# Optimization experiments

Measured on AMD Instinct MI355X. Metric: run time of the kernel, lower is better.

## Reference

```python
import jax, jax.numpy as jnp
import numpy as np

N = 100000
E = 1600000
D_PCA = 50
D_BIO = 64
HID = 32
HEADS = 4
OUT = 50
EPS = 1e-5


def setup_inputs() -> dict:
    key = jax.random.key(0)
    ks = jax.random.split(key, 32)
    g = lambda i, shape, s=0.05: jax.random.normal(ks[i], shape, dtype=jnp.float32) * s
    inp = {
        'x_pca': jax.random.normal(ks[0], (N, D_PCA), dtype=jnp.float32),
        'x_bio': jax.random.normal(ks[1], (N, D_BIO), dtype=jnp.float32),
        'edge_index': jax.random.randint(ks[2], (2, E), 0, N, dtype=jnp.int32),
        # bio encoder: Linear(64,16) -> BN(16) -> ELU -> Linear(16,16) -> ELU
        'bioW1': g(3, (16, D_BIO)), 'biob1': g(4, (16,)),
        'bn0_g': 1.0 + g(5, (16,)), 'bn0_b': g(6, (16,)),
        'bn0_m': g(7, (16,)), 'bn0_v': 1.0 + 0.1 * jax.random.uniform(ks[8], (16,), dtype=jnp.float32),
        'bioW2': g(9, (16, 16)), 'biob2': g(10, (16,)),
        # GATv2 layer 1: in = 50+16 = 66, out = HEADS*HID concat
        'Wl1': g(11, (HEADS * HID, D_PCA + 16)), 'bl1': g(12, (HEADS * HID,)),
        'Wr1': g(13, (HEADS * HID, D_PCA + 16)), 'br1': g(14, (HEADS * HID,)),
        'att1': g(15, (HEADS, HID)), 'bias1': g(16, (HEADS * HID,)),
        'bn1_g': 1.0 + g(17, (HEADS * HID,)), 'bn1_b': g(18, (HEADS * HID,)),
        'bn1_m': g(19, (HEADS * HID,)), 'bn1_v': 1.0 + 0.1 * jax.random.uniform(ks[20], (HEADS * HID,), dtype=jnp.float32),
        # GATv2 layer 2: in = HEADS*HID, heads=1, concat=False
        'Wl2': g(21, (HID, HEADS * HID)), 'bl2': g(22, (HID,)),
        'Wr2': g(23, (HID, HEADS * HID)), 'br2': g(24, (HID,)),
        'att2': g(25, (1, HID)), 'bias2': g(26, (HID,)),
        'bn2_g': 1.0 + g(27, (HID,)), 'bn2_b': g(28, (HID,)),
        'bn2_m': g(29, (HID,)), 'bn2_v': 1.0 + 0.1 * jax.random.uniform(ks[30], (HID,), dtype=jnp.float32),
        'predW': g(31, (OUT, HID)), 'predb': jnp.zeros((OUT,), dtype=jnp.float32),
    }
    return inp


def _bn(h, gm, bt, mean, var):
    # BatchNorm1d in eval mode (running stats)
    return (h - mean) * jax.lax.rsqrt(var + EPS) * gm + bt


def _gatv2(x, src, dst, Wl, bl, Wr, br, att, bias, heads, out_dim, concat):
    n = x.shape[0]
    xl = (x @ Wl.T + bl).reshape(n, heads, out_dim)  # source transform
    xr = (x @ Wr.T + br).reshape(n, heads, out_dim)  # target transform
    e = jax.nn.leaky_relu(xl[src] + xr[dst], 0.2)    # [E,H,C]
    logits = jnp.einsum('ehc,hc->eh', e, att)        # [E,H]
    m = jax.ops.segment_max(logits, dst, num_segments=n)
    a = jnp.exp(logits - m[dst])
    denom = jax.ops.segment_sum(a, dst, num_segments=n)
    alpha = a / (denom[dst] + 1e-16)                 # segment softmax over dst
    out = jax.ops.segment_sum(xl[src] * alpha[..., None], dst, num_segments=n)
    out = out.reshape(n, heads * out_dim) if concat else out.mean(axis=1)
    return out + bias


def reference(x_pca, x_bio, edge_index,
              bioW1, biob1, bn0_g, bn0_b, bn0_m, bn0_v, bioW2, biob2,
              Wl1, bl1, Wr1, br1, att1, bias1, bn1_g, bn1_b, bn1_m, bn1_v,
              Wl2, bl2, Wr2, br2, att2, bias2, bn2_g, bn2_b, bn2_m, bn2_v,
              predW, predb):
    n = x_pca.shape[0]
    # add self-loops (PyG GATv2Conv default)
    loop = jnp.arange(n, dtype=edge_index.dtype)
    src = jnp.concatenate([edge_index[0], loop])
    dst = jnp.concatenate([edge_index[1], loop])

    # bio encoder
    h_bio = jax.nn.elu(_bn(x_bio @ bioW1.T + biob1, bn0_g, bn0_b, bn0_m, bn0_v))
    h_bio = jax.nn.elu(h_bio @ bioW2.T + biob2)
    x = jnp.concatenate([x_pca, h_bio], axis=1)  # [N, 66]

    h = _gatv2(x, src, dst, Wl1, bl1, Wr1, br1, att1, bias1, HEADS, HID, True)
    h = jax.nn.elu(_bn(h, bn1_g, bn1_b, bn1_m, bn1_v))  # dropout off (eval)
    h = _gatv2(h, src, dst, Wl2, bl2, Wr2, br2, att2, bias2, 1, HID, False)
    h = jax.nn.elu(_bn(h, bn2_g, bn2_b, bn2_m, bn2_v))
    return h @ predW.T + predb
```

## Files before the change

kernel.cpp:

```cpp
#include <hip/hip_runtime.h>
#include <hip/hip_fp16.h>
#include <cstdint>
#include <cstddef>

#define NN 100000
#define NE 1600000
#define NEP (NE + NN)
#define NBLK 200
#define CHUNK ((NEP + NBLK - 1) / NBLK)
#define NBUCK2 ((NN + 255) / 256)
#define HISTN (NBUCK2 * NBLK)
#define HSCAN_BLOCKS ((HISTN + 1023) / 1024)

typedef __attribute__((ext_vector_type(8))) _Float16 half8;
typedef __attribute__((ext_vector_type(4))) _Float16 h4v;
typedef __attribute__((ext_vector_type(2))) _Float16 h2v;
typedef __attribute__((ext_vector_type(4))) float float4v;

__device__ __forceinline__ float elu_f(float x) {
    return x > 0.f ? x : __expf(x) - 1.f;
}

template<int CTRL>
__device__ __forceinline__ float dpp_add(float x) {
    int s = __builtin_amdgcn_update_dpp(0, __float_as_int(x), CTRL, 0xF, 0xF, true);
    return x + __int_as_float(s);
}
__device__ __forceinline__ float sum4_all(float x) {
    x = dpp_add<0xB1>(x); x = dpp_add<0x4E>(x);
    return x;
}
__device__ __forceinline__ float sum8_all(float x) {
    x = dpp_add<0xB1>(x); x = dpp_add<0x4E>(x); x = dpp_add<0x141>(x);
    return x;
}

__device__ __forceinline__ float dot2f(h2v a, h2v b, float c) {
#if __has_builtin(__builtin_amdgcn_fdot2)
    return __builtin_amdgcn_fdot2(a, b, c, false);
#else
    return fmaf((float)a[0], (float)b[0], fmaf((float)a[1], (float)b[1], c));
#endif
}

__device__ __forceinline__ h2v hmax2v(h2v a, h2v b) {
#if __has_builtin(__builtin_elementwise_max)
    return __builtin_elementwise_max(a, b);
#else
    __half2 r = __hmax2(*(__half2*)&a, *(__half2*)&b);
    return *(h2v*)&r;
#endif
}


__global__ __launch_bounds__(256) void part_hist(const int* __restrict__ ei, int* __restrict__ hist)
{
    __shared__ int cnt[NBUCK2];
    int tid = threadIdx.x, k = blockIdx.x;
    for (int i = tid; i < NBUCK2; i += 256) cnt[i] = 0;
    __syncthreads();
    int e0 = k * CHUNK, e1 = min(e0 + CHUNK, NEP);
    for (int e = e0 + tid; e < e1; e += 256) {
        int dst = (e < NE) ? ei[NE + e] : e - NE;
        atomicAdd(&cnt[dst >> 8], 1);
    }
    __syncthreads();
    for (int i = tid; i < NBUCK2; i += 256) hist[i * NBLK + k] = cnt[i];
}

__global__ __launch_bounds__(256) void scan_p1(const int* __restrict__ src, int* __restrict__ part, int n)
{
    __shared__ int wsum[4];
    int t = threadIdx.x;
    int i0 = blockIdx.x * 1024 + t * 4;
    int s = 0;
    if (i0 + 3 < n) { int4 d = *(const int4*)(src + i0); s = d.x + d.y + d.z + d.w; }
    else { for (int k = 0; k < 4; k++) if (i0 + k < n) s += src[i0 + k]; }
    for (int d = 1; d < 64; d <<= 1) s += __shfl_xor(s, d, 64);
    if ((t & 63) == 0) wsum[t >> 6] = s;
    __syncthreads();
    if (t == 0) part[blockIdx.x] = wsum[0] + wsum[1] + wsum[2] + wsum[3];
}

__global__ __launch_bounds__(128) void scan_p2(int* __restrict__ part, int nb, int* __restrict__ off)
{
    __shared__ int wt[2];
    int t = threadIdx.x;
    int lane = t & 63, w = t >> 6;
    int v = (t < nb) ? part[t] : 0;
    int x = v;
    for (int d = 1; d < 64; d <<= 1) { int y = __shfl_up(x, d, 64); if (lane >= d) x += y; }
    if (lane == 63) wt[w] = x;
    __syncthreads();
    int base = (w == 1) ? wt[0] : 0;
    int excl = base + x - v;
    if (t < nb) part[t] = excl;
    if (t == 0) off[NN] = NEP;
}

__global__ __launch_bounds__(256) void scan_p3(int* __restrict__ data, const int* __restrict__ part, int n)
{
    __shared__ int wsum[4];
    int t = threadIdx.x, lane = t & 63, w = t >> 6;
    int i0 = blockIdx.x * 1024 + t * 4;
    int d0 = 0, d1 = 0, d2 = 0, d3 = 0;
    if (i0 + 3 < n) { int4 d = *(const int4*)(data + i0); d0 = d.x; d1 = d.y; d2 = d.z; d3 = d.w; }
    else if (i0 < n) {
        d0 = data[i0];
        if (i0 + 1 < n) d1 = data[i0 + 1];
        if (i0 + 2 < n) d2 = data[i0 + 2];
    }
    int s = d0 + d1 + d2 + d3;
    int x = s;
    for (int d = 1; d < 64; d <<= 1) { int y = __shfl_up(x, d, 64); if (lane >= d) x += y; }
    if (lane == 63) wsum[w] = x;
    __syncthreads();
    int wb = 0;
    for (int i = 0; i < w; i++) wb += wsum[i];
    int base = part[blockIdx.x] + wb + x - s;
    if (i0 < n)     data[i0]     = base;
    if (i0 + 1 < n) data[i0 + 1] = base + d0;
    if (i0 + 2 < n) data[i0 + 2] = base + d0 + d1;
    if (i0 + 3 < n) data[i0 + 3] = base + d0 + d1 + d2;
}

__global__ __launch_bounds__(256) void part_scatter(const int* __restrict__ ei,
                                                    const int* __restrict__ hist,
                                                    unsigned* __restrict__ ebuf)
{
    __shared__ int cur[NBUCK2];
    int tid = threadIdx.x, k = blockIdx.x;
    for (int i = tid; i < NBUCK2; i += 256) cur[i] = hist[i * NBLK + k];
    __syncthreads();
    int e0 = k * CHUNK, e1 = min(e0 + CHUNK, NEP);
    for (int e = e0 + tid; e < e1; e += 256) {
        int src, dst;
        if (e < NE) { src = ei[e]; dst = ei[NE + e]; } else { src = dst = e - NE; }
        int pos = atomicAdd(&cur[dst >> 8], 1);
        ebuf[pos] = (unsigned)src | ((unsigned)(dst & 255) << 24);
    }
}

__global__ __launch_bounds__(256) void bucket_csr(const int* __restrict__ hist,
                                                  const unsigned* __restrict__ ebuf,
                                                  int* __restrict__ off, int* __restrict__ csr)
{
    __shared__ int cnt[256];
    __shared__ int cur[256];
    __shared__ int wsum[4];
    int b = blockIdx.x;
    int d0 = b << 8;
    int tid = threadIdx.x;
    int e0 = hist[b * NBLK];
    int e1 = (b + 1 < NBUCK2) ? hist[(b + 1) * NBLK] : NEP;
    cnt[tid] = 0;
    __syncthreads();
    for (int i = e0 + tid; i < e1; i += 256) atomicAdd(&cnt[ebuf[i] >> 24], 1);
    __syncthreads();
    int c = cnt[tid];
    int x = c;
    int lane = tid & 63, w = tid >> 6;
    for (int d = 1; d < 64; d <<= 1) { int y = __shfl_up(x, d, 64); if (lane >= d) x += y; }
    if (lane == 63) wsum[w] = x;
    __syncthreads();
    int wb = 0;
    for (int i = 0; i < w; i++) wb += wsum[i];
    int excl = wb + x - c;
    cur[tid] = e0 + excl;
    int node = d0 + tid;
    if (node < NN) off[node] = e0 + excl;
    __syncthreads();
    for (int i = e0 + tid; i < e1; i += 256) {
        unsigned v = ebuf[i];
        int p = atomicAdd(&cur[v >> 24], 1);
        csr[p] = (int)(v & 0xFFFFFF);
    }
}


__global__ __launch_bounds__(256) void bio_kernel(
    const float* __restrict__ xb, const float* __restrict__ xp,
    const float* __restrict__ W1, const float* __restrict__ b1,
    const float* __restrict__ g0, const float* __restrict__ bb0,
    const float* __restrict__ m0, const float* __restrict__ v0,
    const float* __restrict__ W2, const float* __restrict__ b2,
    __half* __restrict__ xh)
{
    __shared__ float sW1[16*64], sW2[16*16], sb1[16], sb2[16], ss[16], st[16];
    int tid = threadIdx.x;
    for (int idx = tid; idx < 1024; idx += 256) sW1[idx] = W1[idx];
    if (tid < 256) sW2[tid] = W2[tid];
    if (tid < 16) {
        sb1[tid] = b1[tid]; sb2[tid] = b2[tid];
        float s = g0[tid] * rsqrtf(v0[tid] + 1e-5f);
        ss[tid] = s; st[tid] = bb0[tid] - m0[tid] * s;
    }
    __syncthreads();
    int i = blockIdx.x * 256 + tid;
    if (i >= NN) return;
    float bio[64];
    const float4* p = (const float4*)(xb + (size_t)i * 64);
    #pragma unroll
    for (int q = 0; q < 16; q++) {
        float4 f = p[q];
        bio[q*4] = f.x; bio[q*4+1] = f.y; bio[q*4+2] = f.z; bio[q*4+3] = f.w;
    }
    float t1[16];
    #pragma unroll
    for (int j = 0; j < 16; j++) {
        float acc = sb1[j];
        #pragma unroll
        for (int k = 0; k < 64; k++) acc += bio[k] * sW1[j*64 + k];
        acc = acc * ss[j] + st[j];
        t1[j] = elu_f(acc);
    }
    __half* xrow = xh + (size_t)i * 96;
    const float* xpr = xp + (size_t)i * 50;
    #pragma unroll
    for (int j = 0; j < 25; j++) {
        float2 f = *(const float2*)(xpr + 2 * j);
        *(__half2*)(xrow + 2 * j) = __floats2half2_rn(f.x, f.y);
    }
    #pragma unroll
    for (int j = 0; j < 16; j++) {
        float acc = sb2[j];
        #pragma unroll
        for (int k = 0; k < 16; k++) acc += t1[k] * sW2[j*16 + k];
        xrow[50 + j] = __float2half(elu_f(acc));
    }
    __half2 z2 = __floats2half2_rn(0.f, 0.f);
    #pragma unroll
    for (int j = 0; j < 15; j++) *(__half2*)(xrow + 66 + 2 * j) = z2;
}


__global__ __launch_bounds__(256) void wconvert_all(
    const float* __restrict__ Wl1, const float* __restrict__ Wr1,
    const float* __restrict__ bl1, const float* __restrict__ br1,
    const float* __restrict__ Wl2, const float* __restrict__ Wr2,
    const float* __restrict__ bl2, const float* __restrict__ br2,
    const float* __restrict__ predW, const float* __restrict__ predb,
    __half* __restrict__ wcat1, float* __restrict__ bcat1,
    __half* __restrict__ wcat2, float* __restrict__ bcat2,
    __half* __restrict__ wpred, float* __restrict__ bpred)
{
    int t = blockIdx.x * 256 + threadIdx.x;
    if (t < 256 * 96) {
        int j = t / 96, k = t - j * 96;
        float v = (k < 66) ? ((j < 128) ? Wl1[j * 66 + k] : Wr1[(j - 128) * 66 + k]) : 0.f;
        wcat1[t] = __float2half(v);
    }
    int u = t - 256 * 96;
    if (u >= 0 && u < 64 * 128) {
        int j = u >> 7, k = u & 127;
        float v = (j < 32) ? Wl2[j * 128 + k] : Wr2[(j - 32) * 128 + k];
        wcat2[u] = __float2half(v);
    }
    int w = u - 64 * 128;
    if (w >= 0 && w < 64 * 32) {
        int j = w >> 5;
        wpred[w] = __float2half(j < 50 ? predW[w] : 0.f);
    }
    int z = w - 64 * 32;
    if (z >= 0 && z < 256) bcat1[z] = (z < 128) ? bl1[z] : br1[z - 128];
    int z2 = z - 256;
    if (z2 >= 0 && z2 < 64) bcat2[z2] = (z2 < 32) ? bl2[z2] : br2[z2 - 32];
    int z3 = z2 - 64;
    if (z3 >= 0 && z3 < 64) bpred[z3] = (z3 < 50) ? predb[z3] : 0.f;
}

template<int KT, int NC, bool FOUT>
__global__ __launch_bounds__(256) void mfma_gemm(
    const __half* __restrict__ in, const __half* __restrict__ wcat,
    const float* __restrict__ bcat, void* __restrict__ outv, int n, int ncol)
{
    constexpr int K = KT * 32;
    constexpr int KP = K + 8;
    __shared__ __half sW[NC * KP];
    __shared__ __half sX[64 * KP];
    __shared__ float sB[NC];
    int tid = threadIdx.x;
    for (int idx = tid * 8; idx < NC * K; idx += 256 * 8) {
        int r = idx / K, c = idx - r * K;
        *(half8*)(&sW[r * KP + c]) = *(const half8*)(&wcat[r * K + c]);
    }
    for (int idx = tid; idx < NC; idx += 256) sB[idx] = bcat[idx];
    int row0 = blockIdx.x * 64;
    half8 hz = {0, 0, 0, 0, 0, 0, 0, 0};
    for (int idx = tid * 8; idx < 64 * K; idx += 256 * 8) {
        int r = idx / K, c = idx - r * K;
        int gr = row0 + r;
        half8 v = (gr < n) ? *(const half8*)(&in[(size_t)gr * K + c]) : hz;
        *(half8*)(&sX[r * KP + c]) = v;
    }
    __syncthreads();
    int w = tid >> 6, lane = tid & 63;
    int m = lane & 15, quad = lane >> 4;
    half8 a[KT];
    #pragma unroll
    for (int kt = 0; kt < KT; kt++)
        a[kt] = *(const half8*)(&sX[(w * 16 + m) * KP + kt * 32 + quad * 8]);
    #pragma unroll 1
    for (int nt = 0; nt < NC / 16; nt++) {
        float4v acc = {0.f, 0.f, 0.f, 0.f};
        #pragma unroll
        for (int kt = 0; kt < KT; kt++) {
            half8 bfrag = *(const half8*)(&sW[(nt * 16 + m) * KP + kt * 32 + quad * 8]);
            acc = __builtin_amdgcn_mfma_f32_16x16x32_f16(a[kt], bfrag, acc, 0, 0, 0);
        }
        int col = nt * 16 + m;
        float bias = sB[col];
        #pragma unroll
        for (int i = 0; i < 4; i++) {
            int r = row0 + w * 16 + quad * 4 + i;
            if (r < n) {
                if (FOUT) { if (col < ncol) ((float*)outv)[(size_t)r * ncol + col] = acc[i] + bias; }
                else ((__half*)outv)[(size_t)r * NC + col] = __float2half(acc[i] + bias);
            }
        }
    }
}

__global__ __launch_bounds__(256) void fused_gat1(
    const int* __restrict__ off, const int* __restrict__ csr,
    const __half* __restrict__ xcat, const float* __restrict__ att,
    const float* __restrict__ bias, const float* __restrict__ g,
    const float* __restrict__ b, const float* __restrict__ m,
    const float* __restrict__ v, __half* __restrict__ h1)
{
    int wave = threadIdx.x >> 6;
    int lane = threadIdx.x & 63;
    int node = blockIdx.x * 4 + wave;
    if (node >= NN) return;
    int row = lane >> 4;
    int cl  = lane & 15;
    int ch  = cl * 8;

    half8 xr8 = *(const half8*)(xcat + (size_t)node * 256 + 128 + ch);
    float4 af0 = *(const float4*)(att + ch);
    float4 af1 = *(const float4*)(att + ch + 4);
    h2v a01 = {(_Float16)af0.x, (_Float16)af0.y};
    h2v a23 = {(_Float16)af0.z, (_Float16)af0.w};
    h2v a45 = {(_Float16)af1.x, (_Float16)af1.y};
    h2v a67 = {(_Float16)af1.z, (_Float16)af1.w};
    h2v xr01 = {xr8[0], xr8[1]}, xr23 = {xr8[2], xr8[3]};
    h2v xr45 = {xr8[4], xr8[5]}, xr67 = {xr8[6], xr8[7]};
    const h2v c2 = {(_Float16)0.2f, (_Float16)0.2f};

    int k0 = off[node], k1 = off[node + 1];
    float acc0 = 0.f, acc1 = 0.f, acc2 = 0.f, acc3 = 0.f;
    float acc4 = 0.f, acc5 = 0.f, acc6 = 0.f, acc7 = 0.f, denom = 0.f;

    for (int base = k0; base < k1; base += 64) {
        int nb = min(64, k1 - base);
        int mysrc = (lane < nb) ? csr[base + lane] : 0;
        int nbm1 = nb - 1;
        int ss = __shfl(mysrc, min(row, nbm1), 64);
        half8 cur = *(const half8*)(xcat + (size_t)(unsigned)ss * 256 + ch);
        for (int t = 0; t < nb; t += 4) {
            int ns = __shfl(mysrc, min(t + 4 + row, nbm1), 64);
            half8 nxt = *(const half8*)(xcat + (size_t)(unsigned)ns * 256 + ch);

            h2v xl01 = {cur[0], cur[1]}, xl23 = {cur[2], cur[3]};
            h2v xl45 = {cur[4], cur[5]}, xl67 = {cur[6], cur[7]};
            h2v s01 = xl01 + xr01, s23 = xl23 + xr23;
            h2v s45 = xl45 + xr45, s67 = xl67 + xr67;
            h2v l01 = hmax2v(s01, s01 * c2);
            h2v l23 = hmax2v(s23, s23 * c2);
            h2v l45 = hmax2v(s45, s45 * c2);
            h2v l67 = hmax2v(s67, s67 * c2);
            float pp = dot2f(l01, a01, dot2f(l23, a23, dot2f(l45, a45, dot2f(l67, a67, 0.f))));
            pp = sum4_all(pp);
            bool valid = (t + row) < nb;
            float wgt = valid ? __expf(pp) : 0.f;
            denom += wgt;
            acc0 = fmaf((float)cur[0], wgt, acc0);
            acc1 = fmaf((float)cur[1], wgt, acc1);
            acc2 = fmaf((float)cur[2], wgt, acc2);
            acc3 = fmaf((float)cur[3], wgt, acc3);
            acc4 = fmaf((float)cur[4], wgt, acc4);
            acc5 = fmaf((float)cur[5], wgt, acc5);
            acc6 = fmaf((float)cur[6], wgt, acc6);
            acc7 = fmaf((float)cur[7], wgt, acc7);
            cur = nxt;
        }
    }
    acc0 += __shfl_xor(acc0, 16, 64); acc0 += __shfl_xor(acc0, 32, 64);
    acc1 += __shfl_xor(acc1, 16, 64); acc1 += __shfl_xor(acc1, 32, 64);
    acc2 += __shfl_xor(acc2, 16, 64); acc2 += __shfl_xor(acc2, 32, 64);
    acc3 += __shfl_xor(acc3, 16, 64); acc3 += __shfl_xor(acc3, 32, 64);
    acc4 += __shfl_xor(acc4, 16, 64); acc4 += __shfl_xor(acc4, 32, 64);
    acc5 += __shfl_xor(acc5, 16, 64); acc5 += __shfl_xor(acc5, 32, 64);
    acc6 += __shfl_xor(acc6, 16, 64); acc6 += __shfl_xor(acc6, 32, 64);
    acc7 += __shfl_xor(acc7, 16, 64); acc7 += __shfl_xor(acc7, 32, 64);
    denom += __shfl_xor(denom, 16, 64); denom += __shfl_xor(denom, 32, 64);
    if (row == 0) {
        float inv = 1.f / (denom + 1e-16f);
        float4 g0v = *(const float4*)(g + ch),    g1v = *(const float4*)(g + ch + 4);
        float4 v0v = *(const float4*)(v + ch),    v1v = *(const float4*)(v + ch + 4);
        float4 b0v = *(const float4*)(b + ch),    b1v = *(const float4*)(b + ch + 4);
        float4 m0v = *(const float4*)(m + ch),    m1v = *(const float4*)(m + ch + 4);
        float4 i0v = *(const float4*)(bias + ch), i1v = *(const float4*)(bias + ch + 4);
        float sc, o[8];
        sc = g0v.x * rsqrtf(v0v.x + 1e-5f); o[0] = elu_f((acc0 * inv + i0v.x) * sc + (b0v.x - m0v.x * sc));
        sc = g0v.y * rsqrtf(v0v.y + 1e-5f); o[1] = elu_f((acc1 * inv + i0v.y) * sc + (b0v.y - m0v.y * sc));
        sc = g0v.z * rsqrtf(v0v.z + 1e-5f); o[2] = elu_f((acc2 * inv + i0v.z) * sc + (b0v.z - m0v.z * sc));
        sc = g0v.w * rsqrtf(v0v.w + 1e-5f); o[3] = elu_f((acc3 * inv + i0v.w) * sc + (b0v.w - m0v.w * sc));
        sc = g1v.x * rsqrtf(v1v.x + 1e-5f); o[4] = elu_f((acc4 * inv + i1v.x) * sc + (b1v.x - m1v.x * sc));
        sc = g1v.y * rsqrtf(v1v.y + 1e-5f); o[5] = elu_f((acc5 * inv + i1v.y) * sc + (b1v.y - m1v.y * sc));
        sc = g1v.z * rsqrtf(v1v.z + 1e-5f); o[6] = elu_f((acc6 * inv + i1v.z) * sc + (b1v.z - m1v.z * sc));
        sc = g1v.w * rsqrtf(v1v.w + 1e-5f); o[7] = elu_f((acc7 * inv + i1v.w) * sc + (b1v.w - m1v.w * sc));
        half8 oh = {(_Float16)o[0], (_Float16)o[1], (_Float16)o[2], (_Float16)o[3],
                    (_Float16)o[4], (_Float16)o[5], (_Float16)o[6], (_Float16)o[7]};
        *(half8*)(h1 + (size_t)node * 128 + ch) = oh;
    }
}

__global__ __launch_bounds__(256) void fused_gat2(
    const int* __restrict__ off, const int* __restrict__ csr,
    const __half* __restrict__ xcat2, const float* __restrict__ att,
    const float* __restrict__ bias, const float* __restrict__ g,
    const float* __restrict__ b, const float* __restrict__ m,
    const float* __restrict__ v, __half* __restrict__ h2)
{
    int wave = threadIdx.x >> 6;
    int lane = threadIdx.x & 63;
    int node = blockIdx.x * 4 + wave;
    if (node >= NN) return;
    int row = lane >> 3;
    int cl  = lane & 7;
    int ch  = cl * 4;

    h4v xr4 = *(const h4v*)(xcat2 + (size_t)node * 64 + 32 + ch);
    h2v xr01 = {xr4[0], xr4[1]}, xr23 = {xr4[2], xr4[3]};
    float4 af = *(const float4*)(att + ch);
    h2v a01 = {(_Float16)af.x, (_Float16)af.y};
    h2v a23 = {(_Float16)af.z, (_Float16)af.w};
    const h2v c2 = {(_Float16)0.2f, (_Float16)0.2f};

    int k0 = off[node], k1 = off[node + 1];
    float acc0 = 0.f, acc1 = 0.f, acc2 = 0.f, acc3 = 0.f, denom = 0.f;

    for (int base = k0; base < k1; base += 64) {
        int nb = min(64, k1 - base);
        int mysrc = (lane < nb) ? csr[base + lane] : 0;
        int nbm1 = nb - 1;
        int ss = __shfl(mysrc, min(row, nbm1), 64);
        h4v cur = *(const h4v*)(xcat2 + (size_t)(unsigned)ss * 64 + ch);
        for (int t = 0; t < nb; t += 8) {
            int ns = __shfl(mysrc, min(t + 8 + row, nbm1), 64);
            h4v nxt = *(const h4v*)(xcat2 + (size_t)(unsigned)ns * 64 + ch);

            h2v xl01 = {cur[0], cur[1]}, xl23 = {cur[2], cur[3]};
            h2v s01 = xl01 + xr01, s23 = xl23 + xr23;
            h2v l01 = hmax2v(s01, s01 * c2);
            h2v l23 = hmax2v(s23, s23 * c2);
            float pp = dot2f(l01, a01, dot2f(l23, a23, 0.f));
            pp = sum8_all(pp);
            bool valid = (t + row) < nb;
            float wgt = valid ? __expf(pp) : 0.f;
            denom += wgt;
            acc0 = fmaf((float)cur[0], wgt, acc0);
            acc1 = fmaf((float)cur[1], wgt, acc1);
            acc2 = fmaf((float)cur[2], wgt, acc2);
            acc3 = fmaf((float)cur[3], wgt, acc3);
            cur = nxt;
        }
    }
    acc0 += __shfl_xor(acc0, 8, 64); acc0 += __shfl_xor(acc0, 16, 64); acc0 += __shfl_xor(acc0, 32, 64);
    acc1 += __shfl_xor(acc1, 8, 64); acc1 += __shfl_xor(acc1, 16, 64); acc1 += __shfl_xor(acc1, 32, 64);
    acc2 += __shfl_xor(acc2, 8, 64); acc2 += __shfl_xor(acc2, 16, 64); acc2 += __shfl_xor(acc2, 32, 64);
    acc3 += __shfl_xor(acc3, 8, 64); acc3 += __shfl_xor(acc3, 16, 64); acc3 += __shfl_xor(acc3, 32, 64);
    denom += __shfl_xor(denom, 8, 64); denom += __shfl_xor(denom, 16, 64); denom += __shfl_xor(denom, 32, 64);
    if (row == 0) {
        float inv = 1.f / (denom + 1e-16f);
        float4 gv = *(const float4*)(g + ch);
        float4 vv = *(const float4*)(v + ch);
        float4 bv = *(const float4*)(b + ch);
        float4 mv = *(const float4*)(m + ch);
        float4 iv = *(const float4*)(bias + ch);
        float sc, o0, o1, o2, o3;
        sc = gv.x * rsqrtf(vv.x + 1e-5f); o0 = elu_f((acc0 * inv + iv.x) * sc + (bv.x - mv.x * sc));
        sc = gv.y * rsqrtf(vv.y + 1e-5f); o1 = elu_f((acc1 * inv + iv.y) * sc + (bv.y - mv.y * sc));
        sc = gv.z * rsqrtf(vv.z + 1e-5f); o2 = elu_f((acc2 * inv + iv.z) * sc + (bv.z - mv.z * sc));
        sc = gv.w * rsqrtf(vv.w + 1e-5f); o3 = elu_f((acc3 * inv + iv.w) * sc + (bv.w - mv.w * sc));
        h4v oh = {(_Float16)o0, (_Float16)o1, (_Float16)o2, (_Float16)o3};
        *(h4v*)(h2 + (size_t)node * 32 + ch) = oh;
    }
}

extern "C" void kernel_launch(void* const* d_in, const int* in_sizes, int n_in,
                              void* d_out, int out_size, void* d_ws, size_t ws_size,
                              hipStream_t stream)
{
    const float* x_pca = (const float*)d_in[0];
    const float* x_bio = (const float*)d_in[1];
    const int*   ei    = (const int*)d_in[2];
    const float* bioW1 = (const float*)d_in[3];
    const float* biob1 = (const float*)d_in[4];
    const float* bn0_g = (const float*)d_in[5];
    const float* bn0_b = (const float*)d_in[6];
    const float* bn0_m = (const float*)d_in[7];
    const float* bn0_v = (const float*)d_in[8];
    const float* bioW2 = (const float*)d_in[9];
    const float* biob2 = (const float*)d_in[10];
    const float* Wl1   = (const float*)d_in[11];
    const float* bl1   = (const float*)d_in[12];
    const float* Wr1   = (const float*)d_in[13];
    const float* br1   = (const float*)d_in[14];
    const float* att1  = (const float*)d_in[15];
    const float* bias1 = (const float*)d_in[16];
    const float* bn1_g = (const float*)d_in[17];
    const float* bn1_b = (const float*)d_in[18];
    const float* bn1_m = (const float*)d_in[19];
    const float* bn1_v = (const float*)d_in[20];
    const float* Wl2   = (const float*)d_in[21];
    const float* bl2   = (const float*)d_in[22];
    const float* Wr2   = (const float*)d_in[23];
    const float* br2   = (const float*)d_in[24];
    const float* att2  = (const float*)d_in[25];
    const float* bias2 = (const float*)d_in[26];
    const float* bn2_g = (const float*)d_in[27];
    const float* bn2_b = (const float*)d_in[28];
    const float* bn2_m = (const float*)d_in[29];
    const float* bn2_v = (const float*)d_in[30];
    const float* predW = (const float*)d_in[31];
    const float* predb = (const float*)d_in[32];

    float* ws = (float*)d_ws;
    __half* xh    = (__half*)ws;
    float*  p0    = ws + 4800000;
    __half* xcat1 = (__half*)p0;
    float*  p1    = p0 + 12800000;
    __half* h1h   = (__half*)p1;
    float*  p2    = p1 + 6400000;
    __half* xcat2 = (__half*)p2;
    float*  p3    = p2 + 3200000;
    __half* h2h   = (__half*)p3;
    float*  p4    = p3 + 1600000;
    __half* wcat1 = (__half*)p4;
    float*  bcat1 = p4 + 12288;
    __half* wcat2 = (__half*)(bcat1 + 256);
    float*  bcat2 = bcat1 + 256 + 4096;
    __half* wpred = (__half*)(bcat2 + 64);
    float*  bpred = bcat2 + 64 + 1024;
    int*    ib    = (int*)(bpred + 64);
    unsigned* ebuf = (unsigned*)ib;
    int*    hist   = ib + NEP;
    int*    part   = hist + HISTN;
    int*    off    = part + 128;
    int*    csr    = off + NN + 1;

    float* out = (float*)d_out;

    part_hist<<<NBLK, 256, 0, stream>>>(ei, hist);
    scan_p1<<<HSCAN_BLOCKS, 256, 0, stream>>>(hist, part, HISTN);
    scan_p2<<<1, 128, 0, stream>>>(part, HSCAN_BLOCKS, off);
    scan_p3<<<HSCAN_BLOCKS, 256, 0, stream>>>(hist, part, HISTN);
    part_scatter<<<NBLK, 256, 0, stream>>>(ei, hist, ebuf);
    bucket_csr<<<NBUCK2, 256, 0, stream>>>(hist, ebuf, off, csr);

    bio_kernel<<<(NN + 255) / 256, 256, 0, stream>>>(
        x_bio, x_pca, bioW1, biob1, bn0_g, bn0_b, bn0_m, bn0_v, bioW2, biob2, xh);

    wconvert_all<<<138, 256, 0, stream>>>(
        Wl1, Wr1, bl1, br1, Wl2, Wr2, bl2, br2, predW, predb,
        wcat1, bcat1, wcat2, bcat2, wpred, bpred);

    mfma_gemm<3, 256, false><<<(NN + 63) / 64, 256, 0, stream>>>(xh, wcat1, bcat1, xcat1, NN, 0);

    fused_gat1<<<(NN + 3) / 4, 256, 0, stream>>>(
        off, csr, xcat1, att1, bias1, bn1_g, bn1_b, bn1_m, bn1_v, h1h);

    mfma_gemm<4, 64, false><<<(NN + 63) / 64, 256, 0, stream>>>(h1h, wcat2, bcat2, xcat2, NN, 0);

    fused_gat2<<<(NN + 3) / 4, 256, 0, stream>>>(
        off, csr, xcat2, att2, bias2, bn2_g, bn2_b, bn2_m, bn2_v, h2h);

    mfma_gemm<1, 64, true><<<(NN + 63) / 64, 256, 0, stream>>>(h2h, wpred, bpred, out, NN, 50);
}
```

Before: 417.2 us.

## Deepen gather prefetch in GAT edge loops, use exp2, precompute BN affine

```diff
diff --git a/kernel.cpp b/kernel.cpp
--- a/kernel.cpp
+++ b/kernel.cpp
@@ -19,6 +19,14 @@
 
 __device__ __forceinline__ float elu_f(float x) {
     return x > 0.f ? x : __expf(x) - 1.f;
+}
+
+__device__ __forceinline__ float ex2(float x) {
+#if __has_builtin(__builtin_amdgcn_exp2f)
+    return __builtin_amdgcn_exp2f(x);
+#else
+    return exp2f(x);
+#endif
 }
 
 template<int CTRL>
@@ -240,9 +248,17 @@
     const float* __restrict__ Wl2, const float* __restrict__ Wr2,
     const float* __restrict__ bl2, const float* __restrict__ br2,
     const float* __restrict__ predW, const float* __restrict__ predb,
+    const float* __restrict__ bias1, const float* __restrict__ bn1g,
+    const float* __restrict__ bn1b, const float* __restrict__ bn1m,
+    const float* __restrict__ bn1v,
+    const float* __restrict__ bias2, const float* __restrict__ bn2g,
+    const float* __restrict__ bn2b, const float* __restrict__ bn2m,
+    const float* __restrict__ bn2v,
     __half* __restrict__ wcat1, float* __restrict__ bcat1,
     __half* __restrict__ wcat2, float* __restrict__ bcat2,
-    __half* __restrict__ wpred, float* __restrict__ bpred)
+    __half* __restrict__ wpred, float* __restrict__ bpred,
+    float* __restrict__ scb1, float* __restrict__ shb1,
+    float* __restrict__ scb2, float* __restrict__ shb2)
 {
     int t = blockIdx.x * 256 + threadIdx.x;
     if (t < 256 * 96) {
@@ -267,6 +283,18 @@
     if (z2 >= 0 && z2 < 64) bcat2[z2] = (z2 < 32) ? bl2[z2] : br2[z2 - 32];
     int z3 = z2 - 64;
     if (z3 >= 0 && z3 < 64) bpred[z3] = (z3 < 50) ? predb[z3] : 0.f;
+    int z4 = z3 - 64;
+    if (z4 >= 0 && z4 < 128) {
+        float sc = bn1g[z4] * rsqrtf(bn1v[z4] + 1e-5f);
+        scb1[z4] = sc;
+        shb1[z4] = bn1b[z4] + (bias1[z4] - bn1m[z4]) * sc;
+    }
+    int z5 = z4 - 128;
+    if (z5 >= 0 && z5 < 32) {
+        float sc = bn2g[z5] * rsqrtf(bn2v[z5] + 1e-5f);
+        scb2[z5] = sc;
+        shb2[z5] = bn2b[z5] + (bias2[z5] - bn2m[z5]) * sc;
+    }
 }
 
 template<int KT, int NC, bool FOUT>
@@ -324,9 +352,8 @@
 __global__ __launch_bounds__(256) void fused_gat1(
     const int* __restrict__ off, const int* __restrict__ csr,
     const __half* __restrict__ xcat, const float* __restrict__ att,
-    const float* __restrict__ bias, const float* __restrict__ g,
-    const float* __restrict__ b, const float* __restrict__ m,
-    const float* __restrict__ v, __half* __restrict__ h1)
+    const float* __restrict__ scb, const float* __restrict__ shb,
+    __half* __restrict__ h1)
 {
     int wave = threadIdx.x >> 6;
     int lane = threadIdx.x & 63;
@@ -335,14 +362,17 @@
     int row = lane >> 4;
     int cl  = lane & 15;
     int ch  = cl * 8;
-
-    half8 xr8 = *(const half8*)(xcat + (size_t)node * 256 + 128 + ch);
+    unsigned chb = (unsigned)cl * 16u;
+    const char* xbase = (const char*)xcat;
+    const float LOG2E = 1.44269504088896f;
+
+    half8 xr8 = *(const half8*)(xbase + (size_t)node * 512 + 256 + chb);
     float4 af0 = *(const float4*)(att + ch);
     float4 af1 = *(const float4*)(att + ch + 4);
-    h2v a01 = {(_Float16)af0.x, (_Float16)af0.y};
-    h2v a23 = {(_Float16)af0.z, (_Float16)af0.w};
-    h2v a45 = {(_Float16)af1.x, (_Float16)af1.y};
-    h2v a67 = {(_Float16)af1.z, (_Float16)af1.w};
+    h2v a01 = {(_Float16)(af0.x * LOG2E), (_Float16)(af0.y * LOG2E)};
+    h2v a23 = {(_Float16)(af0.z * LOG2E), (_Float16)(af0.w * LOG2E)};
+    h2v a45 = {(_Float16)(af1.x * LOG2E), (_Float16)(af1.y * LOG2E)};
+    h2v a67 = {(_Float16)(af1.z * LOG2E), (_Float16)(af1.w * LOG2E)};
     h2v xr01 = {xr8[0], xr8[1]}, xr23 = {xr8[2], xr8[3]};
     h2v xr45 = {xr8[4], xr8[5]}, xr67 = {xr8[6], xr8[7]};
     const h2v c2 = {(_Float16)0.2f, (_Float16)0.2f};
@@ -351,38 +381,56 @@
     float acc0 = 0.f, acc1 = 0.f, acc2 = 0.f, acc3 = 0.f;
     float acc4 = 0.f, acc5 = 0.f, acc6 = 0.f, acc7 = 0.f, denom = 0.f;
 
+    int rowp4 = row + 4;
+
+    auto edge = [&](half8 cur, bool valid) {
+        h2v xl01 = {cur[0], cur[1]}, xl23 = {cur[2], cur[3]};
+        h2v xl45 = {cur[4], cur[5]}, xl67 = {cur[6], cur[7]};
+        h2v s01 = xl01 + xr01, s23 = xl23 + xr23;
+        h2v s45 = xl45 + xr45, s67 = xl67 + xr67;
+        h2v l01 = hmax2v(s01, s01 * c2);
+        h2v l23 = hmax2v(s23, s23 * c2);
+        h2v l45 = hmax2v(s45, s45 * c2);
+        h2v l67 = hmax2v(s67, s67 * c2);
+        float pp = dot2f(l01, a01, dot2f(l23, a23, dot2f(l45, a45, dot2f(l67, a67, 0.f))));
+        pp = sum4_all(pp);
+        float wgt = valid ? ex2(pp) : 0.f;
+        denom += wgt;
+        acc0 = fmaf((float)cur[0], wgt, acc0);
+        acc1 = fmaf((float)cur[1], wgt, acc1);
+        acc2 = fmaf((float)cur[2], wgt, acc2);
+        acc3 = fmaf((float)cur[3], wgt, acc3);
+        acc4 = fmaf((float)cur[4], wgt, acc4);
+        acc5 = fmaf((float)cur[5], wgt, acc5);
+        acc6 = fmaf((float)cur[6], wgt, acc6);
+        acc7 = fmaf((float)cur[7], wgt, acc7);
+    };
+
     for (int base = k0; base < k1; base += 64) {
         int nb = min(64, k1 - base);
         int mysrc = (lane < nb) ? csr[base + lane] : 0;
-        int nbm1 = nb - 1;
-        int ss = __shfl(mysrc, min(row, nbm1), 64);
-        half8 cur = *(const half8*)(xcat + (size_t)(unsigned)ss * 256 + ch);
-        for (int t = 0; t < nb; t += 4) {
-            int ns = __shfl(mysrc, min(t + 4 + row, nbm1), 64);
-            half8 nxt = *(const half8*)(xcat + (size_t)(unsigned)ns * 256 + ch);
-
-            h2v xl01 = {cur[0], cur[1]}, xl23 = {cur[2], cur[3]};
-            h2v xl45 = {cur[4], cur[5]}, xl67 = {cur[6], cur[7]};
-            h2v s01 = xl01 + xr01, s23 = xl23 + xr23;
-            h2v s45 = xl45 + xr45, s67 = xl67 + xr67;
-            h2v l01 = hmax2v(s01, s01 * c2);
-            h2v l23 = hmax2v(s23, s23 * c2);
-            h2v l45 = hmax2v(s45, s45 * c2);
-            h2v l67 = hmax2v(s67, s67 * c2);
-            float pp = dot2f(l01, a01, dot2f(l23, a23, dot2f(l45, a45, dot2f(l67, a67, 0.f))));
-            pp = sum4_all(pp);
-            bool valid = (t + row) < nb;
-            float wgt = valid ? __expf(pp) : 0.f;
-            denom += wgt;
-            acc0 = fmaf((float)cur[0], wgt, acc0);
-            acc1 = fmaf((float)cur[1], wgt, acc1);
-            acc2 = fmaf((float)cur[2], wgt, acc2);
-            acc3 = fmaf((float)cur[3], wgt, acc3);
-            acc4 = fmaf((float)cur[4], wgt, acc4);
-            acc5 = fmaf((float)cur[5], wgt, acc5);
-            acc6 = fmaf((float)cur[6], wgt, acc6);
-            acc7 = fmaf((float)cur[7], wgt, acc7);
-            cur = nxt;
+        int pairs = (nb + 7) >> 3;
+
+        auto loadpair = [&](half8& A, half8& B, int j) {
+            int i0 = __shfl(mysrc, j * 8 + row, 64);
+            int i1 = __shfl(mysrc, j * 8 + rowp4, 64);
+            A = *(const half8*)(xbase + (((unsigned)i0 << 9) + chb));
+            B = *(const half8*)(xbase + (((unsigned)i1 << 9) + chb));
+        };
+        auto edgepair = [&](half8 A, half8 B, int j) {
+            edge(A, (j * 8 + row) < nb);
+            edge(B, (j * 8 + rowp4) < nb);
+        };
+
+        half8 A0, B0, A1, B1, A2, B2;
+        loadpair(A0, B0, 0);
+        if (pairs > 1) loadpair(A1, B1, 1);
+        if (pairs > 2) loadpair(A2, B2, 2);
+        int j = 0;
+        while (true) {
+            edgepair(A0, B0, j); if (j + 3 < pairs) loadpair(A0, B0, j + 3); if (++j >= pairs) break;
+            edgepair(A1, B1, j); if (j + 3 < pairs) loadpair(A1, B1, j + 3); if (++j >= pairs) break;
+            edgepair(A2, B2, j); if (j + 3 < pairs) loadpair(A2, B2, j + 3); if (++j >= pairs) break;
         }
     }
     acc0 += __shfl_xor(acc0, 16, 64); acc0 += __shfl_xor(acc0, 32, 64);
@@ -396,20 +444,17 @@
     denom += __shfl_xor(denom, 16, 64); denom += __shfl_xor(denom, 32, 64);
     if (row == 0) {
         float inv = 1.f / (denom + 1e-16f);
-        float4 g0v = *(const float4*)(g + ch),    g1v = *(const float4*)(g + ch + 4);
-        float4 v0v = *(const float4*)(v + ch),    v1v = *(const float4*)(v + ch + 4);
-        float4 b0v = *(const float4*)(b + ch),    b1v = *(const float4*)(b + ch + 4);
-        float4 m0v = *(const float4*)(m + ch),    m1v = *(const float4*)(m + ch + 4);
-        float4 i0v = *(const float4*)(bias + ch), i1v = *(const float4*)(bias + ch + 4);
-        float sc, o[8];
-        sc = g0v.x * rsqrtf(v0v.x + 1e-5f); o[0] = elu_f((acc0 * inv + i0v.x) * sc + (b0v.x - m0v.x * sc));
-        sc = g0v.y * rsqrtf(v0v.y + 1e-5f); o[1] = elu_f((acc1 * inv + i0v.y) * sc + (b0v.y - m0v.y * sc));
-        sc = g0v.z * rsqrtf(v0v.z + 1e-5f); o[2] = elu_f((acc2 * inv + i0v.z) * sc + (b0v.z - m0v.z * sc));
-        sc = g0v.w * rsqrtf(v0v.w + 1e-5f); o[3] = elu_f((acc3 * inv + i0v.w) * sc + (b0v.w - m0v.w * sc));
-        sc = g1v.x * rsqrtf(v1v.x + 1e-5f); o[4] = elu_f((acc4 * inv + i1v.x) * sc + (b1v.x - m1v.x * sc));
-        sc = g1v.y * rsqrtf(v1v.y + 1e-5f); o[5] = elu_f((acc5 * inv + i1v.y) * sc + (b1v.y - m1v.y * sc));
-        sc = g1v.z * rsqrtf(v1v.z + 1e-5f); o[6] = elu_f((acc6 * inv + i1v.z) * sc + (b1v.z - m1v.z * sc));
-        sc = g1v.w * rsqrtf(v1v.w + 1e-5f); o[7] = elu_f((acc7 * inv + i1v.w) * sc + (b1v.w - m1v.w * sc));
+        float4 s0 = *(const float4*)(scb + ch), s1 = *(const float4*)(scb + ch + 4);
+        float4 h0 = *(const float4*)(shb + ch), h1f = *(const float4*)(shb + ch + 4);
+        float o[8];
+        o[0] = elu_f(fmaf(acc0 * inv, s0.x, h0.x));
+        o[1] = elu_f(fmaf(acc1 * inv, s0.y, h0.y));
+        o[2] = elu_f(fmaf(acc2 * inv, s0.z, h0.z));
+        o[3] = elu_f(fmaf(acc3 * inv, s0.w, h0.w));
+        o[4] = elu_f(fmaf(acc4 * inv, s1.x, h1f.x));
+        o[5] = elu_f(fmaf(acc5 * inv, s1.y, h1f.y));
+        o[6] = elu_f(fmaf(acc6 * inv, s1.z, h1f.z));
+        o[7] = elu_f(fmaf(acc7 * inv, s1.w, h1f.w));
         half8 oh = {(_Float16)o[0], (_Float16)o[1], (_Float16)o[2], (_Float16)o[3],
                     (_Float16)o[4], (_Float16)o[5], (_Float16)o[6], (_Float16)o[7]};
         *(half8*)(h1 + (size_t)node * 128 + ch) = oh;
@@ -419,9 +464,8 @@
 __global__ __launch_bounds__(256) void fused_gat2(
     const int* __restrict__ off, const int* __restrict__ csr,
     const __half* __restrict__ xcat2, const float* __restrict__ att,
-    const float* __restrict__ bias, const float* __restrict__ g,
-    const float* __restrict__ b, const float* __restrict__ m,
-    const float* __restrict__ v, __half* __restrict__ h2)
+    const float* __restrict__ scb, const float* __restrict__ shb,
+    __half* __restrict__ h2)
 {
     int wave = threadIdx.x >> 6;
     int lane = threadIdx.x & 63;
@@ -430,41 +474,62 @@
     int row = lane >> 3;
     int cl  = lane & 7;
     int ch  = cl * 4;
-
-    h4v xr4 = *(const h4v*)(xcat2 + (size_t)node * 64 + 32 + ch);
+    unsigned chb = (unsigned)cl * 8u;
+    const char* xbase = (const char*)xcat2;
+    const float LOG2E = 1.44269504088896f;
+
+    h4v xr4 = *(const h4v*)(xbase + (size_t)node * 128 + 64 + chb);
     h2v xr01 = {xr4[0], xr4[1]}, xr23 = {xr4[2], xr4[3]};
     float4 af = *(const float4*)(att + ch);
-    h2v a01 = {(_Float16)af.x, (_Float16)af.y};
-    h2v a23 = {(_Float16)af.z, (_Float16)af.w};
+    h2v a01 = {(_Float16)(af.x * LOG2E), (_Float16)(af.y * LOG2E)};
+    h2v a23 = {(_Float16)(af.z * LOG2E), (_Float16)(af.w * LOG2E)};
     const h2v c2 = {(_Float16)0.2f, (_Float16)0.2f};
 
     int k0 = off[node], k1 = off[node + 1];
     float acc0 = 0.f, acc1 = 0.f, acc2 = 0.f, acc3 = 0.f, denom = 0.f;
+
+    int rowp8 = row + 8;
+
+    auto edge = [&](h4v cur, bool valid) {
+        h2v xl01 = {cur[0], cur[1]}, xl23 = {cur[2], cur[3]};
+        h2v s01 = xl01 + xr01, s23 = xl23 + xr23;
+        h2v l01 = hmax2v(s01, s01 * c2);
+        h2v l23 = hmax2v(s23, s23 * c2);
+        float pp = dot2f(l01, a01, dot2f(l23, a23, 0.f));
+        pp = sum8_all(pp);
+        float wgt = valid ? ex2(pp) : 0.f;
+        denom += wgt;
+        acc0 = fmaf((float)cur[0], wgt, acc0);
+        acc1 = fmaf((float)cur[1], wgt, acc1);
+        acc2 = fmaf((float)cur[2], wgt, acc2);
+        acc3 = fmaf((float)cur[3], wgt, acc3);
+    };
 
     for (int base = k0; base < k1; base += 64) {
         int nb = min(64, k1 - base);
         int mysrc = (lane < nb) ? csr[base + lane] : 0;
-        int nbm1 = nb - 1;
-        int ss = __shfl(mysrc, min(row, nbm1), 64);
-        h4v cur = *(const h4v*)(xcat2 + (size_t)(unsigned)ss * 64 + ch);
-        for (int t = 0; t < nb; t += 8) {
-            int ns = __shfl(mysrc, min(t + 8 + row, nbm1), 64);
-            h4v nxt = *(const h4v*)(xcat2 + (size_t)(unsigned)ns * 64 + ch);
-
-            h2v xl01 = {cur[0], cur[1]}, xl23 = {cur[2], cur[3]};
-            h2v s01 = xl01 + xr01, s23 = xl23 + xr23;
-            h2v l01 = hmax2v(s01, s01 * c2);
-            h2v l23 = hmax2v(s23, s23 * c2);
-            float pp = dot2f(l01, a01, dot2f(l23, a23, 0.f));
-            pp = sum8_all(pp);
-            bool valid = (t + row) < nb;
-            float wgt = valid ? __expf(pp) : 0.f;
-            denom += wgt;
-            acc0 = fmaf((float)cur[0], wgt, acc0);
-            acc1 = fmaf((float)cur[1], wgt, acc1);
-            acc2 = fmaf((float)cur[2], wgt, acc2);
-            acc3 = fmaf((float)cur[3], wgt, acc3);
-            cur = nxt;
+        int pairs = (nb + 15) >> 4;
+
+        auto loadpair = [&](h4v& A, h4v& B, int j) {
+            int i0 = __shfl(mysrc, j * 16 + row, 64);
+            int i1 = __shfl(mysrc, j * 16 + rowp8, 64);
+            A = *(const h4v*)(xbase + (((unsigned)i0 << 7) + chb));
+            B = *(const h4v*)(xbase + (((unsigned)i1 << 7) + chb));
+        };
+        auto edgepair = [&](h4v A, h4v B, int j) {
+            edge(A, (j * 16 + row) < nb);
+            edge(B, (j * 16 + rowp8) < nb);
+        };
+
+        h4v A0, B0, A1, B1, A2, B2;
+        loadpair(A0, B0, 0);
+        if (pairs > 1) loadpair(A1, B1, 1);
+        if (pairs > 2) loadpair(A2, B2, 2);
+        int j = 0;
+        while (true) {
+            edgepair(A0, B0, j); if (j + 3 < pairs) loadpair(A0, B0, j + 3); if (++j >= pairs) break;
+            edgepair(A1, B1, j); if (j + 3 < pairs) loadpair(A1, B1, j + 3); if (++j >= pairs) break;
+            edgepair(A2, B2, j); if (j + 3 < pairs) loadpair(A2, B2, j + 3); if (++j >= pairs) break;
         }
     }
     acc0 += __shfl_xor(acc0, 8, 64); acc0 += __shfl_xor(acc0, 16, 64); acc0 += __shfl_xor(acc0, 32, 64);
@@ -474,16 +539,12 @@
     denom += __shfl_xor(denom, 8, 64); denom += __shfl_xor(denom, 16, 64); denom += __shfl_xor(denom, 32, 64);
     if (row == 0) {
         float inv = 1.f / (denom + 1e-16f);
-        float4 gv = *(const float4*)(g + ch);
-        float4 vv = *(const float4*)(v + ch);
-        float4 bv = *(const float4*)(b + ch);
-        float4 mv = *(const float4*)(m + ch);
-        float4 iv = *(const float4*)(bias + ch);
-        float sc, o0, o1, o2, o3;
-        sc = gv.x * rsqrtf(vv.x + 1e-5f); o0 = elu_f((acc0 * inv + iv.x) * sc + (bv.x - mv.x * sc));
-        sc = gv.y * rsqrtf(vv.y + 1e-5f); o1 = elu_f((acc1 * inv + iv.y) * sc + (bv.y - mv.y * sc));
-        sc = gv.z * rsqrtf(vv.z + 1e-5f); o2 = elu_f((acc2 * inv + iv.z) * sc + (bv.z - mv.z * sc));
-        sc = gv.w * rsqrtf(vv.w + 1e-5f); o3 = elu_f((acc3 * inv + iv.w) * sc + (bv.w - mv.w * sc));
+        float4 sv = *(const float4*)(scb + ch);
+        float4 hv = *(const float4*)(shb + ch);
+        float o0 = elu_f(fmaf(acc0 * inv, sv.x, hv.x));
+        float o1 = elu_f(fmaf(acc1 * inv, sv.y, hv.y));
+        float o2 = elu_f(fmaf(acc2 * inv, sv.z, hv.z));
+        float o3 = elu_f(fmaf(acc3 * inv, sv.w, hv.w));
         h4v oh = {(_Float16)o0, (_Float16)o1, (_Float16)o2, (_Float16)o3};
         *(h4v*)(h2 + (size_t)node * 32 + ch) = oh;
     }
@@ -544,7 +605,11 @@
     float*  bcat2 = bcat1 + 256 + 4096;
     __half* wpred = (__half*)(bcat2 + 64);
     float*  bpred = bcat2 + 64 + 1024;
-    int*    ib    = (int*)(bpred + 64);
+    float*  scb1  = bpred + 64;
+    float*  shb1  = scb1 + 128;
+    float*  scb2  = shb1 + 128;
+    float*  shb2  = scb2 + 32;
+    int*    ib    = (int*)(shb2 + 32);
     unsigned* ebuf = (unsigned*)ib;
     int*    hist   = ib + NEP;
     int*    part   = hist + HISTN;
@@ -563,19 +628,22 @@
     bio_kernel<<<(NN + 255) / 256, 256, 0, stream>>>(
         x_bio, x_pca, bioW1, biob1, bn0_g, bn0_b, bn0_m, bn0_v, bioW2, biob2, xh);
 
-    wconvert_all<<<138, 256, 0, stream>>>(
+    wconvert_all<<<139, 256, 0, stream>>>(
         Wl1, Wr1, bl1, br1, Wl2, Wr2, bl2, br2, predW, predb,
-        wcat1, bcat1, wcat2, bcat2, wpred, bpred);
+        bias1, bn1_g, bn1_b, bn1_m, bn1_v,
+        bias2, bn2_g, bn2_b, bn2_m, bn2_v,
+        wcat1, bcat1, wcat2, bcat2, wpred, bpred,
+        scb1, shb1, scb2, shb2);
 
     mfma_gemm<3, 256, false><<<(NN + 63) / 64, 256, 0, stream>>>(xh, wcat1, bcat1, xcat1, NN, 0);
 
     fused_gat1<<<(NN + 3) / 4, 256, 0, stream>>>(
-        off, csr, xcat1, att1, bias1, bn1_g, bn1_b, bn1_m, bn1_v, h1h);
+        off, csr, xcat1, att1, scb1, shb1, h1h);
 
     mfma_gemm<4, 64, false><<<(NN + 63) / 64, 256, 0, stream>>>(h1h, wcat2, bcat2, xcat2, NN, 0);
 
     fused_gat2<<<(NN + 3) / 4, 256, 0, stream>>>(
-        off, csr, xcat2, att2, bias2, bn2_g, bn2_b, bn2_m, bn2_v, h2h);
+        off, csr, xcat2, att2, scb2, shb2, h2h);
 
     mfma_gemm<1, 64, true><<<(NN + 63) / 64, 256, 0, stream>>>(h2h, wpred, bpred, out, NN, 50);
 }
```

Measured after the change: 413.2 us. About the same (-1.0%).
